# Optimization experiments

Measured on AMD Instinct MI355X. Metric: run time of the kernel, lower is better.

The kernel has to match this reference:

```python
import jax, jax.numpy as jnp
import numpy as np
import math

B, T, C = 2, 2048, 1024
H = 16
D = C // H


def setup_inputs() -> dict:
    key = jax.random.key(0)
    ks = jax.random.split(key, 5)
    s = 1.0 / math.sqrt(C)
    return {
        "x": jax.random.normal(ks[0], (B, T, C), dtype=jnp.float32),
        "W_qkv": jax.random.normal(ks[1], (C, 3 * C), dtype=jnp.float32) * s,
        "b_qkv": jnp.zeros((3 * C,), dtype=jnp.float32),
        "W_proj": jax.random.normal(ks[2], (C, C), dtype=jnp.float32) * s,
        "b_proj": jnp.zeros((C,), dtype=jnp.float32),
    }


def reference(x, W_qkv, b_qkv, W_proj, b_proj):
    qkv = x @ W_qkv + b_qkv  # [B,T,3C]
    q, k, v = jnp.split(qkv, 3, axis=-1)
    # [B,T,C] -> [B,H,T,D]
    q = q.reshape(B, T, H, D).transpose(0, 2, 1, 3)
    k = k.reshape(B, T, H, D).transpose(0, 2, 1, 3)
    v = v.reshape(B, T, H, D).transpose(0, 2, 1, 3)
    sm_scale = 1.0 / math.sqrt(D)
    att = jnp.einsum("bhqd,bhkd->bhqk", q, k) * sm_scale
    causal = jnp.tril(jnp.ones((T, T), dtype=bool))  # True = keep
    att = jnp.where(causal, att, -jnp.inf)
    att = jax.nn.softmax(att, axis=-1)
    y = jnp.einsum("bhqk,bhkd->bhqd", att, v)  # [B,H,T,D]
    y = y.transpose(0, 2, 1, 3).reshape(B, T, C)
    return y @ W_proj + b_proj
```

## Files before the change

kernel.cpp:

```cpp
#include <hip/hip_runtime.h>
#include <hip/hip_bf16.h>
#include <math.h>

#define BB 2
#define TT 2048
#define CCH 1024
#define HH 16
#define DD 64
#define BT (BB*TT)
#define N3 (3*CCH)

typedef __attribute__((ext_vector_type(8))) short short8;
typedef __attribute__((ext_vector_type(4))) float f32x4;
typedef __attribute__((ext_vector_type(16))) float f32x16;

__device__ __forceinline__ unsigned short f2bf(float f) {
  unsigned int u = __float_as_uint(f);
  unsigned int r = (u + 0x7FFFu + ((u >> 16) & 1u)) >> 16;
  return (unsigned short)r;
}
__device__ __forceinline__ int cvtpk(float lo, float hi) {
  int r;
  asm("v_cvt_pk_bf16_f32 %0, %1, %2" : "=v"(r) : "v"(lo), "v"(hi));
  return r;
}
__device__ __forceinline__ void plswap(int &a, int &b) {
  asm("v_permlane32_swap_b32 %0, %1" : "+v"(a), "+v"(b));
}
__device__ __forceinline__ float fexp2(float x) {
  float r;
  asm("v_exp_f32 %0, %1" : "=v"(r) : "v"(x));
  return r;
}
__device__ __forceinline__ void gload_lds16(const unsigned short* g, unsigned short* l) {
  __builtin_amdgcn_global_load_lds((const __attribute__((address_space(1))) void*)g,
                                   (__attribute__((address_space(3))) void*)l, 16, 0, 0);
}
__device__ __forceinline__ float fmax3(float a, float b, float c) {
  return fmaxf(fmaxf(a, b), c);
}

__global__ __launch_bounds__(256) void k_convert(const float* __restrict__ in,
                                                 unsigned short* __restrict__ out, int n8) {
  int i = blockIdx.x * 256 + threadIdx.x;
  if (i < n8) {
    const float4 a = *(const float4*)(in + (size_t)i * 8);
    const float4 b = *(const float4*)(in + (size_t)i * 8 + 4);
    short8 v;
    v[0] = f2bf(a.x); v[1] = f2bf(a.y); v[2] = f2bf(a.z); v[3] = f2bf(a.w);
    v[4] = f2bf(b.x); v[5] = f2bf(b.y); v[6] = f2bf(b.z); v[7] = f2bf(b.w);
    *(short8*)(out + (size_t)i * 8) = v;
  }
}

__global__ __launch_bounds__(256) void k_transpose_cvt(const float* __restrict__ in,
                                                       unsigned short* __restrict__ out,
                                                       int R, int Cn) {
  __shared__ float tile[32][33];
  int tc = blockIdx.x * 32;
  int tr = blockIdx.y * 32;
  int lx = threadIdx.x & 31;
  int ly = threadIdx.x >> 5;
#pragma unroll
  for (int i = 0; i < 32; i += 8)
    tile[ly + i][lx] = in[(size_t)(tr + ly + i) * Cn + tc + lx];
  __syncthreads();
#pragma unroll
  for (int i = 0; i < 32; i += 8)
    out[(size_t)(tc + ly + i) * R + tr + lx] = f2bf(tile[lx][ly + i]);
}

__global__ __launch_bounds__(256) void k_qkv_gemm(const unsigned short* __restrict__ Xb,
                                                  const unsigned short* __restrict__ Wt,
                                                  const float* __restrict__ bias,
                                                  unsigned short* __restrict__ Qo,
                                                  unsigned short* __restrict__ Ko,
                                                  unsigned short* __restrict__ Vto) {
  __shared__ __align__(16) unsigned short As[128 * 32];
  __shared__ __align__(16) unsigned short Bs[128 * 32];
  int tid = threadIdx.x;
  int mb = blockIdx.x * 128;
  int nb = blockIdx.y * 128;
  int wid = tid >> 6, lane = tid & 63;
  int wr = (wid >> 1) * 64, wc = (wid & 1) * 64;
  int l15 = lane & 15, l4 = lane >> 4;
  int l16 = lane >> 2, lc = (lane & 3) * 8;
  f32x4 acc[4][4];
#pragma unroll
  for (int a = 0; a < 4; ++a)
#pragma unroll
    for (int b = 0; b < 4; ++b)
#pragma unroll
      for (int j = 0; j < 4; ++j) acc[a][b][j] = 0.0f;

  for (int kb = 0; kb < CCH; kb += 32) {
#pragma unroll
    for (int i = 0; i < 2; ++i) {
      int arow = wid * 32 + i * 16;
      gload_lds16(Xb + (size_t)(mb + arow + l16) * CCH + kb + lc, &As[arow * 32]);
      gload_lds16(Wt + (size_t)(nb + arow + l16) * CCH + kb + lc, &Bs[arow * 32]);
    }
    __syncthreads();
    short8 af[4], bfr[4];
#pragma unroll
    for (int mt = 0; mt < 4; ++mt) af[mt] = *(const short8*)(&As[(wr + mt * 16 + l15) * 32 + l4 * 8]);
#pragma unroll
    for (int nt = 0; nt < 4; ++nt) bfr[nt] = *(const short8*)(&Bs[(wc + nt * 16 + l15) * 32 + l4 * 8]);
#pragma unroll
    for (int mt = 0; mt < 4; ++mt)
#pragma unroll
      for (int nt = 0; nt < 4; ++nt)
        acc[mt][nt] = __builtin_amdgcn_mfma_f32_16x16x32_bf16(af[mt], bfr[nt], acc[mt][nt], 0, 0, 0);
    __syncthreads();
  }

#pragma unroll
  for (int mt = 0; mt < 4; ++mt) {
#pragma unroll
    for (int nt = 0; nt < 4; ++nt) {
      int gcol = nb + wc + nt * 16 + l15;
      int which = gcol >> 10;
      int cc = gcol & 1023;
      int h = cc >> 6, d = cc & 63;
      float bv = bias[gcol];
#pragma unroll
      for (int j = 0; j < 4; ++j) {
        int grow = mb + wr + mt * 16 + l4 * 4 + j;
        int b = grow >> 11, t = grow & 2047;
        float v = acc[mt][nt][j] + bv;
        size_t bh = (size_t)(b * HH + h);
        if (which == 0)      Qo[(bh * TT + t) * DD + d] = f2bf(v * 0.18033688f);
        else if (which == 1) Ko[(bh * TT + t) * DD + d] = f2bf(v);
        else                 Vto[(bh * DD + d) * TT + t] = f2bf(v);
      }
    }
  }
}

__global__ __launch_bounds__(128) void k_attn(const unsigned short* __restrict__ Qb,
                                              const unsigned short* __restrict__ Kb,
                                              const unsigned short* __restrict__ Vtb,
                                              unsigned short* __restrict__ Y) {
  __shared__ __align__(16) unsigned short Ks[2][64 * 64];
  __shared__ __align__(16) unsigned short Vs[2][64 * 64];
  int tid = threadIdx.x;
  int jx = blockIdx.x;
  int j = 63 - (jx >> 5);
  int bh = jx & 31;
  int wid = tid >> 6, lane = tid & 63;
  int l31 = lane & 31, h = lane >> 5;
  int q0 = j * 32;
  int qrow = q0 + l31;
  int tmax = j >> 1;

  const unsigned short* Qp = Qb + (size_t)bh * TT * DD;
  const unsigned short* Kp = Kb + (size_t)bh * TT * DD;
  const unsigned short* Vp = Vtb + (size_t)bh * DD * TT;

  short8 qf[4];
#pragma unroll
  for (int m = 0; m < 4; ++m)
    qf[m] = *(const short8*)(Qp + (size_t)qrow * DD + m * 16 + h * 8);

  f32x16 zv;
#pragma unroll
  for (int r = 0; r < 16; ++r) zv[r] = 0.0f;
  f32x16 po[2];
  po[0] = zv; po[1] = zv;
  float mrun = -1e30f, lrun = 0.0f;

  if (wid <= tmax) {
#pragma unroll
    for (int i = 0; i < 8; ++i) {
      int c = i * 64 + lane;
      int srow = c >> 3, scol = ((c & 7) ^ (srow & 7)) * 8;
      gload_lds16(Kp + (size_t)(wid * 64 + srow) * DD + scol, &Ks[wid][i * 512]);
      gload_lds16(Vp + (size_t)srow * TT + wid * 64 + scol, &Vs[wid][i * 512]);
    }
  }

  for (int t = wid; t <= tmax; t += 2) {
    int kvb = t * 64;
    asm volatile("s_waitcnt vmcnt(0)" ::: "memory");
    __builtin_amdgcn_sched_barrier(0);

    short8 kf[2][4];
#pragma unroll
    for (int t32 = 0; t32 < 2; ++t32) {
      int row = t32 * 32 + l31;
#pragma unroll
      for (int m = 0; m < 4; ++m)
        kf[t32][m] = *(const short8*)(&Ks[wid][row * 64 + (((2 * m + h) ^ (row & 7)) * 8)]);
    }
    f32x16 st[2];
    __builtin_amdgcn_s_setprio(1);
#pragma unroll
    for (int t32 = 0; t32 < 2; ++t32) {
      st[t32] = __builtin_amdgcn_mfma_f32_32x32x16_bf16(kf[t32][0], qf[0], zv, 0, 0, 0);
#pragma unroll
      for (int m = 1; m < 4; ++m)
        st[t32] = __builtin_amdgcn_mfma_f32_32x32x16_bf16(kf[t32][m], qf[m], st[t32], 0, 0, 0);
    }
    __builtin_amdgcn_s_setprio(0);

    short8 vf[2][4];
#pragma unroll
    for (int dt = 0; dt < 2; ++dt) {
      int row = dt * 32 + l31;
#pragma unroll
      for (int g = 0; g < 4; ++g)
        vf[dt][g] = *(const short8*)(&Vs[wid][row * 64 + (((2 * g + h) ^ (row & 7)) * 8)]);
    }
    asm volatile("s_waitcnt lgkmcnt(0)" ::: "memory");
    __builtin_amdgcn_sched_barrier(0);

    if (t + 2 <= tmax) {
      int kvb2 = kvb + 128;
#pragma unroll
      for (int i = 0; i < 8; ++i) {
        int c = i * 64 + lane;
        int srow = c >> 3, scol = ((c & 7) ^ (srow & 7)) * 8;
        gload_lds16(Kp + (size_t)(kvb2 + srow) * DD + scol, &Ks[wid][i * 512]);
        gload_lds16(Vp + (size_t)srow * TT + kvb2 + scol, &Vs[wid][i * 512]);
      }
    }

    if (kvb + 63 > q0) {
#pragma unroll
      for (int t32 = 0; t32 < 2; ++t32)
#pragma unroll
        for (int r = 0; r < 16; ++r) {
          int kvg = kvb + t32 * 32 + (r & 3) + 8 * (r >> 2) + 4 * h;
          if (kvg > qrow) st[t32][r] = -1e30f;
        }
    }

    float A = st[0][0], B = st[0][1], C = st[0][2], Dv = st[0][3];
#pragma unroll
    for (int r = 4; r < 16; r += 4) {
      A = fmax3(A, st[0][r], st[0][r + 1]);
      B = fmax3(B, st[0][r + 2], st[0][r + 3]);
      C = fmax3(C, st[1][r - 4], st[1][r - 3]);
      Dv = fmax3(Dv, st[1][r - 2], st[1][r - 1]);
    }
    C = fmax3(C, st[1][12], st[1][13]);
    Dv = fmax3(Dv, st[1][14], st[1][15]);
    float mx = fmaxf(fmax3(A, B, C), Dv);
    mx = fmaxf(mx, __shfl_xor(mx, 32));

    if (__any(mx - mrun > 8.0f)) {
      float mnew = fmaxf(mrun, mx);
      float alpha = fexp2(mrun - mnew);
      lrun *= alpha;
#pragma unroll
      for (int dt = 0; dt < 2; ++dt)
#pragma unroll
        for (int r = 0; r < 16; ++r) po[dt][r] *= alpha;
      mrun = mnew;
    }

    float sum = 0.0f;
#pragma unroll
    for (int t32 = 0; t32 < 2; ++t32)
#pragma unroll
      for (int r = 0; r < 16; ++r) {
        float p = fexp2(st[t32][r] - mrun);
        st[t32][r] = p;
        sum += p;
      }
    sum += __shfl_xor(sum, 32);
    lrun += sum;

    short8 pf[4];
#pragma unroll
    for (int g = 0; g < 4; ++g) {
      int t32 = g >> 1, r0 = (g & 1) * 8;
      int a = cvtpk(st[t32][r0 + 0], st[t32][r0 + 1]);
      int b = cvtpk(st[t32][r0 + 4], st[t32][r0 + 5]);
      plswap(a, b);
      int c = cvtpk(st[t32][r0 + 2], st[t32][r0 + 3]);
      int d = cvtpk(st[t32][r0 + 6], st[t32][r0 + 7]);
      plswap(c, d);
      union { int w[4]; short8 s; } un;
      un.w[0] = a; un.w[1] = c; un.w[2] = b; un.w[3] = d;
      pf[g] = un.s;
    }

    __builtin_amdgcn_s_setprio(1);
#pragma unroll
    for (int dt = 0; dt < 2; ++dt)
#pragma unroll
      for (int g = 0; g < 4; ++g)
        po[dt] = __builtin_amdgcn_mfma_f32_32x32x16_bf16(vf[dt][g], pf[g], po[dt], 0, 0, 0);
    __builtin_amdgcn_s_setprio(0);
  }

  asm volatile("s_waitcnt vmcnt(0)" ::: "memory");
  __syncthreads();
  float* ex   = (float*)&Ks[0][0];
  float* exml = (float*)&Vs[0][0];
  if (wid == 1) {
#pragma unroll
    for (int dt = 0; dt < 2; ++dt)
#pragma unroll
      for (int r = 0; r < 16; ++r) ex[lane * 33 + dt * 16 + r] = po[dt][r];
    exml[lane] = mrun;
    exml[64 + lane] = lrun;
  }
  __syncthreads();
  if (wid == 0) {
    float m1 = exml[lane], l1 = exml[64 + lane];
    float M = fmaxf(mrun, m1);
    float a0 = fexp2(mrun - M), a1 = fexp2(m1 - M);
    float inv = 1.0f / (lrun * a0 + l1 * a1);
    a0 *= inv; a1 *= inv;
    int b = bh >> 4, hh = bh & 15;
    unsigned short* yp = Y + ((size_t)(b * TT + qrow)) * CCH + hh * DD;
#pragma unroll
    for (int dt = 0; dt < 2; ++dt)
#pragma unroll
      for (int r = 0; r < 16; r += 2) {
        int d = dt * 32 + (r & 3) + 8 * (r >> 2) + 4 * h;
        float v0 = po[dt][r]     * a0 + ex[lane * 33 + dt * 16 + r]     * a1;
        float v1 = po[dt][r + 1] * a0 + ex[lane * 33 + dt * 16 + r + 1] * a1;
        *(int*)(yp + d) = cvtpk(v0, v1);
      }
  }
}

__global__ __launch_bounds__(256) void k_proj_gemm(const unsigned short* __restrict__ Yb,
                                                   const unsigned short* __restrict__ Wt,
                                                   const float* __restrict__ bias,
                                                   float* __restrict__ Out) {
  __shared__ __align__(16) unsigned short As[128 * 32];
  __shared__ __align__(16) unsigned short Bs[128 * 32];
  int tid = threadIdx.x;
  int mb = blockIdx.x * 128;
  int nb = blockIdx.y * 128;
  int wid = tid >> 6, lane = tid & 63;
  int wr = (wid >> 1) * 64, wc = (wid & 1) * 64;
  int l15 = lane & 15, l4 = lane >> 4;
  int l16 = lane >> 2, lc = (lane & 3) * 8;
  f32x4 acc[4][4];
#pragma unroll
  for (int a = 0; a < 4; ++a)
#pragma unroll
    for (int b = 0; b < 4; ++b)
#pragma unroll
      for (int j = 0; j < 4; ++j) acc[a][b][j] = 0.0f;

  for (int kb = 0; kb < CCH; kb += 32) {
#pragma unroll
    for (int i = 0; i < 2; ++i) {
      int arow = wid * 32 + i * 16;
      gload_lds16(Yb + (size_t)(mb + arow + l16) * CCH + kb + lc, &As[arow * 32]);
      gload_lds16(Wt + (size_t)(nb + arow + l16) * CCH + kb + lc, &Bs[arow * 32]);
    }
    __syncthreads();
    short8 af[4], bfr[4];
#pragma unroll
    for (int mt = 0; mt < 4; ++mt) af[mt] = *(const short8*)(&As[(wr + mt * 16 + l15) * 32 + l4 * 8]);
#pragma unroll
    for (int nt = 0; nt < 4; ++nt) bfr[nt] = *(const short8*)(&Bs[(wc + nt * 16 + l15) * 32 + l4 * 8]);
#pragma unroll
    for (int mt = 0; mt < 4; ++mt)
#pragma unroll
      for (int nt = 0; nt < 4; ++nt)
        acc[mt][nt] = __builtin_amdgcn_mfma_f32_16x16x32_bf16(af[mt], bfr[nt], acc[mt][nt], 0, 0, 0);
    __syncthreads();
  }

#pragma unroll
  for (int mt = 0; mt < 4; ++mt) {
#pragma unroll
    for (int nt = 0; nt < 4; ++nt) {
      int gcol = nb + wc + nt * 16 + l15;
      float bv = bias[gcol];
#pragma unroll
      for (int j = 0; j < 4; ++j) {
        int grow = mb + wr + mt * 16 + l4 * 4 + j;
        Out[(size_t)grow * CCH + gcol] = acc[mt][nt][j] + bv;
      }
    }
  }
}

extern "C" void kernel_launch(void* const* d_in, const int* in_sizes, int n_in,
                              void* d_out, int out_size, void* d_ws, size_t ws_size,
                              hipStream_t stream) {
  const float* x      = (const float*)d_in[0];
  const float* W_qkv  = (const float*)d_in[1];
  const float* b_qkv  = (const float*)d_in[2];
  const float* W_proj = (const float*)d_in[3];
  const float* b_proj = (const float*)d_in[4];
  float* out = (float*)d_out;

  char* ws = (char*)d_ws;
  size_t off = 0;
  unsigned short* Wt_qkv  = (unsigned short*)(ws + off); off += (size_t)N3 * CCH * 2;
  unsigned short* Wt_proj = (unsigned short*)(ws + off); off += (size_t)CCH * CCH * 2;
  unsigned short* Xb      = (unsigned short*)(ws + off); off += (size_t)BT * CCH * 2;
  unsigned short* Qb      = (unsigned short*)(ws + off); off += (size_t)BT * CCH * 2;
  unsigned short* Kb      = (unsigned short*)(ws + off); off += (size_t)BT * CCH * 2;
  unsigned short* Vt      = (unsigned short*)(ws + off); off += (size_t)BT * CCH * 2;
  unsigned short* Yb      = (unsigned short*)(ws + off); off += (size_t)BT * CCH * 2;

  k_convert<<<dim3(BT * CCH / 8 / 256), 256, 0, stream>>>(x, Xb, BT * CCH / 8);
  k_transpose_cvt<<<dim3(N3 / 32, CCH / 32), 256, 0, stream>>>(W_qkv, Wt_qkv, CCH, N3);
  k_transpose_cvt<<<dim3(CCH / 32, CCH / 32), 256, 0, stream>>>(W_proj, Wt_proj, CCH, CCH);
  k_qkv_gemm<<<dim3(BT / 128, N3 / 128), 256, 0, stream>>>(Xb, Wt_qkv, b_qkv, Qb, Kb, Vt);
  k_attn<<<dim3(2048), 128, 0, stream>>>(Qb, Kb, Vt, Yb);
  k_proj_gemm<<<dim3(BT / 128, CCH / 128), 256, 0, stream>>>(Yb, Wt_proj, b_proj, out);
}
```

Measured before the change: 120.4 us.

## Store Q/K/V in MFMA fragment order and load attention operands directly from global

The QKV GEMM epilogue now writes Q, K and V in a pre-swizzled layout that matches the MFMA operand fragments, so each lane's 16-byte fragment is contiguous. The attention kernel drops its LDS staging and the double-buffered global-to-LDS prefetch, reading K/V fragments straight from global memory with coalesced 16-byte loads. This removes LDS traffic and waitcnt synchronisation. In exchange it loses explicit prefetch overlap, so global latency is exposed each iteration unless the compiler hoists the loads, and the GEMM epilogue now does more scattered stores.

After: 109.4 us. -9.1%, faster.

```diff
diff --git a/kernel.cpp b/kernel.cpp
--- a/kernel.cpp
+++ b/kernel.cpp
@@ -39,6 +39,7 @@
 __device__ __forceinline__ float fmax3(float a, float b, float c) {
   return fmaxf(fmaxf(a, b), c);
 }
+
 
 __global__ __launch_bounds__(256) void k_convert(const float* __restrict__ in,
                                                  unsigned short* __restrict__ out, int n8) {
@@ -73,9 +74,9 @@
 __global__ __launch_bounds__(256) void k_qkv_gemm(const unsigned short* __restrict__ Xb,
                                                   const unsigned short* __restrict__ Wt,
                                                   const float* __restrict__ bias,
-                                                  unsigned short* __restrict__ Qo,
-                                                  unsigned short* __restrict__ Ko,
-                                                  unsigned short* __restrict__ Vto) {
+                                                  unsigned short* __restrict__ Qf,
+                                                  unsigned short* __restrict__ Kf,
+                                                  unsigned short* __restrict__ Vf) {
   __shared__ __align__(16) unsigned short As[128 * 32];
   __shared__ __align__(16) unsigned short Bs[128 * 32];
   int tid = threadIdx.x;
@@ -121,28 +122,35 @@
       int gcol = nb + wc + nt * 16 + l15;
       int which = gcol >> 10;
       int cc = gcol & 1023;
-      int h = cc >> 6, d = cc & 63;
+      int hh = cc >> 6, d = cc & 63;
       float bv = bias[gcol];
 #pragma unroll
       for (int j = 0; j < 4; ++j) {
         int grow = mb + wr + mt * 16 + l4 * 4 + j;
         int b = grow >> 11, t = grow & 2047;
         float v = acc[mt][nt][j] + bv;
-        size_t bh = (size_t)(b * HH + h);
-        if (which == 0)      Qo[(bh * TT + t) * DD + d] = f2bf(v * 0.18033688f);
-        else if (which == 1) Ko[(bh * TT + t) * DD + d] = f2bf(v);
-        else                 Vto[(bh * DD + d) * TT + t] = f2bf(v);
+        size_t bh = (size_t)(b * HH + hh) * TT * DD;
+        if (which == 2) {
+          size_t a = (size_t)((((t >> 6) * 2 + (d >> 5)) * 4 + ((t >> 4) & 3)) * 512
+                             + (((t >> 3) & 1) * 32 + (d & 31)) * 8 + (t & 7));
+          Vf[bh + a] = f2bf(v);
+        } else {
+          size_t a = (size_t)(((t >> 5) * 4 + (d >> 4)) * 512
+                             + ((d >> 3) & 1) * 256 + (t & 31) * 8 + (d & 7));
+          if (which == 0) Qf[bh + a] = f2bf(v * 0.18033688f);
+          else            Kf[bh + a] = f2bf(v);
+        }
       }
     }
   }
 }
 
-__global__ __launch_bounds__(128) void k_attn(const unsigned short* __restrict__ Qb,
-                                              const unsigned short* __restrict__ Kb,
-                                              const unsigned short* __restrict__ Vtb,
+__global__ __launch_bounds__(128) void k_attn(const unsigned short* __restrict__ Qf,
+                                              const unsigned short* __restrict__ Kf,
+                                              const unsigned short* __restrict__ Vf,
                                               unsigned short* __restrict__ Y) {
-  __shared__ __align__(16) unsigned short Ks[2][64 * 64];
-  __shared__ __align__(16) unsigned short Vs[2][64 * 64];
+  __shared__ float ex[64 * 33];
+  __shared__ float exml[128];
   int tid = threadIdx.x;
   int jx = blockIdx.x;
   int j = 63 - (jx >> 5);
@@ -153,14 +161,14 @@
   int qrow = q0 + l31;
   int tmax = j >> 1;
 
-  const unsigned short* Qp = Qb + (size_t)bh * TT * DD;
-  const unsigned short* Kp = Kb + (size_t)bh * TT * DD;
-  const unsigned short* Vp = Vtb + (size_t)bh * DD * TT;
+  const unsigned short* Qp = Qf + (size_t)bh * TT * DD;
+  const unsigned short* Kp = Kf + (size_t)bh * TT * DD;
+  const unsigned short* Vp = Vf + (size_t)bh * TT * DD;
 
   short8 qf[4];
 #pragma unroll
   for (int m = 0; m < 4; ++m)
-    qf[m] = *(const short8*)(Qp + (size_t)qrow * DD + m * 16 + h * 8);
+    qf[m] = *(const short8*)(Qp + (size_t)(j * 4 + m) * 512 + lane * 8);
 
   f32x16 zv;
 #pragma unroll
@@ -169,29 +177,16 @@
   po[0] = zv; po[1] = zv;
   float mrun = -1e30f, lrun = 0.0f;
 
-  if (wid <= tmax) {
-#pragma unroll
-    for (int i = 0; i < 8; ++i) {
-      int c = i * 64 + lane;
-      int srow = c >> 3, scol = ((c & 7) ^ (srow & 7)) * 8;
-      gload_lds16(Kp + (size_t)(wid * 64 + srow) * DD + scol, &Ks[wid][i * 512]);
-      gload_lds16(Vp + (size_t)srow * TT + wid * 64 + scol, &Vs[wid][i * 512]);
-    }
-  }
-
   for (int t = wid; t <= tmax; t += 2) {
     int kvb = t * 64;
-    asm volatile("s_waitcnt vmcnt(0)" ::: "memory");
-    __builtin_amdgcn_sched_barrier(0);
 
     short8 kf[2][4];
 #pragma unroll
-    for (int t32 = 0; t32 < 2; ++t32) {
-      int row = t32 * 32 + l31;
+    for (int t32 = 0; t32 < 2; ++t32)
 #pragma unroll
       for (int m = 0; m < 4; ++m)
-        kf[t32][m] = *(const short8*)(&Ks[wid][row * 64 + (((2 * m + h) ^ (row & 7)) * 8)]);
-    }
+        kf[t32][m] = *(const short8*)(Kp + (size_t)((t * 2 + t32) * 4 + m) * 512 + lane * 8);
+
     f32x16 st[2];
     __builtin_amdgcn_s_setprio(1);
 #pragma unroll
@@ -205,25 +200,10 @@
 
     short8 vf[2][4];
 #pragma unroll
-    for (int dt = 0; dt < 2; ++dt) {
-      int row = dt * 32 + l31;
+    for (int dt = 0; dt < 2; ++dt)
 #pragma unroll
       for (int g = 0; g < 4; ++g)
-        vf[dt][g] = *(const short8*)(&Vs[wid][row * 64 + (((2 * g + h) ^ (row & 7)) * 8)]);
-    }
-    asm volatile("s_waitcnt lgkmcnt(0)" ::: "memory");
-    __builtin_amdgcn_sched_barrier(0);
-
-    if (t + 2 <= tmax) {
-      int kvb2 = kvb + 128;
-#pragma unroll
-      for (int i = 0; i < 8; ++i) {
-        int c = i * 64 + lane;
-        int srow = c >> 3, scol = ((c & 7) ^ (srow & 7)) * 8;
-        gload_lds16(Kp + (size_t)(kvb2 + srow) * DD + scol, &Ks[wid][i * 512]);
-        gload_lds16(Vp + (size_t)srow * TT + kvb2 + scol, &Vs[wid][i * 512]);
-      }
-    }
+        vf[dt][g] = *(const short8*)(Vp + (size_t)((t * 2 + dt) * 4 + g) * 512 + lane * 8);
 
     if (kvb + 63 > q0) {
 #pragma unroll
@@ -295,10 +275,7 @@
     __builtin_amdgcn_s_setprio(0);
   }
 
-  asm volatile("s_waitcnt vmcnt(0)" ::: "memory");
   __syncthreads();
-  float* ex   = (float*)&Ks[0][0];
-  float* exml = (float*)&Vs[0][0];
   if (wid == 1) {
 #pragma unroll
     for (int dt = 0; dt < 2; ++dt)
@@ -400,15 +377,15 @@
   unsigned short* Wt_qkv  = (unsigned short*)(ws + off); off += (size_t)N3 * CCH * 2;
   unsigned short* Wt_proj = (unsigned short*)(ws + off); off += (size_t)CCH * CCH * 2;
   unsigned short* Xb      = (unsigned short*)(ws + off); off += (size_t)BT * CCH * 2;
-  unsigned short* Qb      = (unsigned short*)(ws + off); off += (size_t)BT * CCH * 2;
-  unsigned short* Kb      = (unsigned short*)(ws + off); off += (size_t)BT * CCH * 2;
-  unsigned short* Vt      = (unsigned short*)(ws + off); off += (size_t)BT * CCH * 2;
+  unsigned short* Qfb     = (unsigned short*)(ws + off); off += (size_t)BT * CCH * 2;
+  unsigned short* Kfb     = (unsigned short*)(ws + off); off += (size_t)BT * CCH * 2;
+  unsigned short* Vfb     = (unsigned short*)(ws + off); off += (size_t)BT * CCH * 2;
   unsigned short* Yb      = (unsigned short*)(ws + off); off += (size_t)BT * CCH * 2;
 
   k_convert<<<dim3(BT * CCH / 8 / 256), 256, 0, stream>>>(x, Xb, BT * CCH / 8);
   k_transpose_cvt<<<dim3(N3 / 32, CCH / 32), 256, 0, stream>>>(W_qkv, Wt_qkv, CCH, N3);
   k_transpose_cvt<<<dim3(CCH / 32, CCH / 32), 256, 0, stream>>>(W_proj, Wt_proj, CCH, CCH);
-  k_qkv_gemm<<<dim3(BT / 128, N3 / 128), 256, 0, stream>>>(Xb, Wt_qkv, b_qkv, Qb, Kb, Vt);
-  k_attn<<<dim3(2048), 128, 0, stream>>>(Qb, Kb, Vt, Yb);
+  k_qkv_gemm<<<dim3(BT / 128, N3 / 128), 256, 0, stream>>>(Xb, Wt_qkv, b_qkv, Qfb, Kfb, Vfb);
+  k_attn<<<dim3(2048), 128, 0, stream>>>(Qfb, Kfb, Vfb, Yb);
   k_proj_gemm<<<dim3(BT / 128, CCH / 128), 256, 0, stream>>>(Yb, Wt_proj, b_proj, out);
 }
```
